# Kernel tuning notes

Measured on AMD Instinct MI355X. Metric: run time of the kernel, lower is better.

Reference implementation:

```python
import jax, jax.numpy as jnp
import numpy as np
from jax import lax

B, N, SEG, T = 64, 19, 15, 400
FIN, HID, K, NH, DM, FF, L, NC = 64, 128, 4, 4, 64, 128, 4, 3
EPS = 1e-5


def setup_inputs() -> dict:
    key = jax.random.key(0)
    ks = jax.random.split(key, 40)
    nrm = lambda i, s, sc=0.05: jax.random.normal(ks[i], s, dtype=jnp.float32) * sc
    inp = {
        "X": jax.random.normal(ks[0], (B, N, SEG, T), dtype=jnp.float32),
        "A_hat": jax.random.uniform(ks[1], (B, K, SEG, N, N), dtype=jnp.float32),
        "conv1_w": nrm(2, (32, 1, 25)), "conv1_b": nrm(3, (32,)),
        "conv2_w": nrm(4, (64, 32, 9)), "conv2_b": nrm(5, (64,)),
        "g1_W": nrm(6, (HID, FIN)), "g1_q": nrm(7, (K,), 1.0),
        "g1_bn_g": jnp.ones((HID,)), "g1_bn_b": jnp.zeros((HID,)),
        "g1_bn_m": jnp.zeros((HID,)), "g1_bn_v": jnp.ones((HID,)),
        "g2_W": nrm(8, (FIN, HID)), "g2_q": nrm(9, (K,), 1.0),
        "g2_bn_g": jnp.ones((FIN,)), "g2_bn_b": jnp.zeros((FIN,)),
        "g2_bn_m": jnp.zeros((FIN,)), "g2_bn_v": jnp.ones((FIN,)),
        "cls_token": nrm(10, (1, 1, DM), 0.02), "pos_emb": nrm(11, (1, SEG + 1, DM), 0.02),
        "t_wqkv": nrm(12, (L, 3 * DM, DM)), "t_bqkv": nrm(13, (L, 3 * DM)),
        "t_wo": nrm(14, (L, DM, DM)), "t_bo": nrm(15, (L, DM)),
        "t_ln1g": jnp.ones((L, DM)), "t_ln1b": jnp.zeros((L, DM)),
        "t_w1": nrm(16, (L, FF, DM)), "t_b1": nrm(17, (L, FF)),
        "t_w2": nrm(18, (L, DM, FF)), "t_b2": nrm(19, (L, DM)),
        "t_ln2g": jnp.ones((L, DM)), "t_ln2b": jnp.zeros((L, DM)),
        "clf_w": nrm(20, (NC, DM)), "clf_b": nrm(21, (NC,)),
    }
    return inp


def _ln(x, g, b):
    mu = x.mean(-1, keepdims=True)
    v = ((x - mu) ** 2).mean(-1, keepdims=True)
    return (x - mu) * lax.rsqrt(v + EPS) * g + b


def _maxpool(x, w):  # x: [M, C, T]
    return lax.reduce_window(x, -jnp.inf, lax.max, (1, 1, w), (1, 1, w), "VALID")


def _temporal_encoder(X, c1w, c1b, c2w, c2b):
    # X: [B, SEG, N, T] -> [B, SEG, N, FIN]
    x = X.reshape(-1, 1, T)
    dn = ("NCH", "OIH", "NCH")
    x = lax.conv_general_dilated(x, c1w, (4,), [(12, 12)], dimension_numbers=dn) + c1b[None, :, None]
    x = _maxpool(jax.nn.relu(x), 4)                      # [M,32,25]
    x = lax.conv_general_dilated(x, c2w, (2,), [(4, 4)], dimension_numbers=dn) + c2b[None, :, None]
    x = _maxpool(jax.nn.relu(x), 2)                      # [M,64,6]
    x = x.mean(-1)                                       # AdaptiveAvgPool1d(1)
    return x.reshape(B, SEG, N, FIN)


def _gcn(Xf, A, W, q, g, b, m, v):
    alpha = jax.nn.softmax(q)                            # [K]
    AX = jnp.einsum("bksnm,bsmf->bksnf", A, Xf)          # K-hop diffusion
    Hk = jnp.einsum("bksnf,of->bksno", AX, W)            # shared linear
    H = jnp.einsum("k,bksno->bsno", alpha, Hk)           # attn-weighted hop mix
    H = (H - m) * lax.rsqrt(v + EPS) * g + b             # eval-mode BatchNorm1d
    return jax.nn.relu(H)


def _forward(X, A_hat, conv1_w, conv1_b, conv2_w, conv2_b,
             g1_W, g1_q, g1_bn_g, g1_bn_b, g1_bn_m, g1_bn_v,
             g2_W, g2_q, g2_bn_g, g2_bn_b, g2_bn_m, g2_bn_v,
             cls_token, pos_emb, t_wqkv, t_bqkv, t_wo, t_bo,
             t_ln1g, t_ln1b, t_w1, t_b1, t_w2, t_b2, t_ln2g, t_ln2b,
             clf_w, clf_b):
    Xs = X.reshape(-1, N, SEG, T).transpose(0, 2, 1, 3)  # [B,SEG,N,T]
    feat = _temporal_encoder(Xs, conv1_w, conv1_b, conv2_w, conv2_b)
    H = _gcn(feat, A_hat, g1_W, g1_q, g1_bn_g, g1_bn_b, g1_bn_m, g1_bn_v)
    H = _gcn(H, A_hat, g2_W, g2_q, g2_bn_g, g2_bn_b, g2_bn_m, g2_bn_v)
    g = H.mean(axis=2)                                   # node-mean -> [B,SEG,DM]
    x = jnp.concatenate([jnp.broadcast_to(cls_token, (B, 1, DM)), g], axis=1)
    x = x + pos_emb[:, : SEG + 1]
    dh = DM // NH
    for l in range(L):
        qkv = x @ t_wqkv[l].T + t_bqkv[l]
        qh, kh, vh = [u.reshape(B, SEG + 1, NH, dh).transpose(0, 2, 1, 3)
                      for u in jnp.split(qkv, 3, axis=-1)]
        attn = jax.nn.softmax(jnp.einsum("bhqd,bhkd->bhqk", qh, kh) / jnp.sqrt(jnp.float32(dh)), axis=-1)
        o = jnp.einsum("bhqk,bhkd->bhqd", attn, vh).transpose(0, 2, 1, 3).reshape(B, SEG + 1, DM)
        x = _ln(x + o @ t_wo[l].T + t_bo[l], t_ln1g[l], t_ln1b[l])
        ff = jax.nn.relu(x @ t_w1[l].T + t_b1[l]) @ t_w2[l].T + t_b2[l]
        x = _ln(x + ff, t_ln2g[l], t_ln2b[l])
    return x[:, 0] @ clf_w.T + clf_b                     # [B, NC]


def reference(X, A_hat, conv1_w, conv1_b, conv2_w, conv2_b,
              g1_W, g1_q, g1_bn_g, g1_bn_b, g1_bn_m, g1_bn_v,
              g2_W, g2_q, g2_bn_g, g2_bn_b, g2_bn_m, g2_bn_v,
              cls_token, pos_emb, t_wqkv, t_bqkv, t_wo, t_bo,
              t_ln1g, t_ln1b, t_w1, t_b1, t_w2, t_b2, t_ln2g, t_ln2b,
              clf_w, clf_b):
    return _forward(X, A_hat, conv1_w, conv1_b, conv2_w, conv2_b,
                    g1_W, g1_q, g1_bn_g, g1_bn_b, g1_bn_m, g1_bn_v,
                    g2_W, g2_q, g2_bn_g, g2_bn_b, g2_bn_m, g2_bn_v,
                    cls_token, pos_emb, t_wqkv, t_bqkv, t_wo, t_bo,
                    t_ln1g, t_ln1b, t_w1, t_b1, t_w2, t_b2, t_ln2g, t_ln2b,
                    clf_w, clf_b)
```

## Files before the change

### kernel.cpp

```cpp
#include <hip/hip_runtime.h>
#include <cmath>

#define B_ 64
#define N_ 19
#define SEG_ 15
#define T_ 400
#define FIN_ 64
#define HID_ 128
#define K_ 4
#define NH_ 4
#define DM_ 64
#define FF_ 128
#define L_ 4
#define NC_ 3
#define EPS_ 1e-5f

typedef __attribute__((ext_vector_type(8))) short bf16x8;
typedef __attribute__((ext_vector_type(4))) short bf16x4;
typedef __attribute__((ext_vector_type(4))) float f32x4;
typedef unsigned short ushort_t;

__device__ __forceinline__ ushort_t f2bf(float x) {
  union { float f; unsigned u; } a; a.f = x;
  unsigned r = a.u + 0x7fffu + ((a.u >> 16) & 1u);
  return (ushort_t)(r >> 16);
}
__device__ __forceinline__ float bf2f(ushort_t h) {
  union { unsigned u; float f; } a; a.u = ((unsigned)h) << 16;
  return a.f;
}

__global__ __launch_bounds__(256) void k_prep(
    const float* __restrict__ c1w, const float* __restrict__ c2w,
    const float* __restrict__ wqkv, const float* __restrict__ wo,
    const float* __restrict__ w1, const float* __restrict__ w2,
    const float* __restrict__ g1W, const float* __restrict__ g2W,
    ushort_t* __restrict__ bt,
    ushort_t* __restrict__ Th, ushort_t* __restrict__ Tl,
    ushort_t* __restrict__ W1h, ushort_t* __restrict__ W1l,
    ushort_t* __restrict__ W2h, ushort_t* __restrict__ W2l,
    ushort_t* __restrict__ C1h, ushort_t* __restrict__ C1l) {
  int gid = blockIdx.x * 256 + threadIdx.x;
  if (gid < 18944) {
    int oc = gid / 296, k = gid - oc * 296;
    int ic = k & 31, kk = k >> 5;
    ushort_t v = 0;
    if (kk < 9) v = f2bf(c2w[oc * 288 + ic * 9 + kk]);
    bt[gid] = v;
  } else if (gid < 68096) {
    int i = gid - 18944;
    int l = i / 12288, r = i % 12288;
    float v = wqkv[i];
    ushort_t h = f2bf(v);
    int dst = l * 32768 + r;
    Th[dst] = h; Tl[dst] = f2bf(v - bf2f(h));
  } else if (gid < 84480) {
    int i = gid - 68096;
    int l = i / 4096, r = i % 4096;
    float v = wo[i];
    ushort_t h = f2bf(v);
    int dst = l * 32768 + 12288 + r;
    Th[dst] = h; Tl[dst] = f2bf(v - bf2f(h));
  } else if (gid < 117248) {
    int i = gid - 84480;
    int l = i / 8192, r = i % 8192;
    float v = w1[i];
    ushort_t h = f2bf(v);
    int dst = l * 32768 + 16384 + r;
    Th[dst] = h; Tl[dst] = f2bf(v - bf2f(h));
  } else if (gid < 150016) {
    int i = gid - 117248;
    int l = i / 8192, r = i % 8192;
    float v = w2[i];
    ushort_t h = f2bf(v);
    int dst = l * 32768 + 24576 + r;
    Th[dst] = h; Tl[dst] = f2bf(v - bf2f(h));
  } else if (gid < 158208) {
    int i = gid - 150016;
    float v = g1W[i];
    ushort_t h = f2bf(v);
    W1h[i] = h;
    W1l[i] = f2bf(v - bf2f(h));
  } else if (gid < 166400) {
    int i = gid - 158208;
    float v = g2W[i];
    ushort_t h = f2bf(v);
    W2h[i] = h;
    W2l[i] = f2bf(v - bf2f(h));
  } else if (gid < 167424) {
    int i = gid - 166400;
    int oc = i >> 5, kk = i & 31;
    float v = (kk < 25) ? c1w[oc * 25 + kk] : 0.f;
    ushort_t h = f2bf(v);
    C1h[i] = h;
    C1l[i] = f2bf(v - bf2f(h));
  }
}

#define RPB 4
#define ICP 40
#define P1R 40
#define OFF_XPH 0
#define OFF_XPL 3840
#define OFF_P1  7680
#define SMEM_T  20480

__global__ __launch_bounds__(256, 4) void k_temporal(
    const float* __restrict__ X, const float* __restrict__ c1b,
    const float* __restrict__ c2b,
    const ushort_t* __restrict__ C1h, const ushort_t* __restrict__ C1l,
    const ushort_t* __restrict__ BmatT, float* __restrict__ Xf) {
  __shared__ __align__(16) unsigned char smem[SMEM_T];
  ushort_t* xph = (ushort_t*)(smem + OFF_XPH);
  ushort_t* xpl = (ushort_t*)(smem + OFF_XPL);
  ushort_t* p1T = (ushort_t*)(smem + OFF_P1);
  float* Dbuf = (float*)smem;

  const int tid = threadIdx.x;
  const int row0 = blockIdx.x * RPB;
  const int lane = tid & 63, wv = tid >> 6;
  const int quad = lane >> 4, nl = lane & 15;

  for (int i = tid; i < 3200; i += 256) ((unsigned*)p1T)[i] = 0u;
  for (int r = 0; r < RPB; ++r) {
    const int gr = row0 + r;
    const int n = gr % N_;
    const int s = (gr / N_) % SEG_;
    const int b = gr / (N_ * SEG_);
    const float* xin = X + (((size_t)b * N_ + n) * SEG_ + s) * T_ - 12;
    for (int i = tid; i < 480; i += 256) {
      float v = (i >= 12 && i < 412) ? xin[i] : 0.f;
      ushort_t h = f2bf(v);
      xph[r * 480 + i] = h;
      xpl[r * 480 + i] = f2bf(v - bf2f(h));
    }
  }
  __syncthreads();

  {
    bf16x8 bh0 = *(const bf16x8*)(C1h + nl * 32 + quad * 8);
    bf16x8 bh1 = *(const bf16x8*)(C1h + (16 + nl) * 32 + quad * 8);
    bf16x8 bl0 = *(const bf16x8*)(C1l + nl * 32 + quad * 8);
    bf16x8 bl1 = *(const bf16x8*)(C1l + (16 + nl) * 32 + quad * 8);
    const float bias0 = c1b[nl], bias1 = c1b[16 + nl];
    for (int t = wv; t < 28; t += 4) {
      const int r = t / 7, mt = t - r * 7;
      const int aoff = r * 480 + mt * 64 + nl * 4 + quad * 8;
      union { bf16x4 q[2]; bf16x8 v; } ah, al;
      ah.q[0] = *(const bf16x4*)(xph + aoff);
      ah.q[1] = *(const bf16x4*)(xph + aoff + 4);
      al.q[0] = *(const bf16x4*)(xpl + aoff);
      al.q[1] = *(const bf16x4*)(xpl + aoff + 4);
      f32x4 a0 = (f32x4){0.f, 0.f, 0.f, 0.f};
      a0 = __builtin_amdgcn_mfma_f32_16x16x32_bf16(ah.v, bh0, a0, 0, 0, 0);
      a0 = __builtin_amdgcn_mfma_f32_16x16x32_bf16(al.v, bh0, a0, 0, 0, 0);
      a0 = __builtin_amdgcn_mfma_f32_16x16x32_bf16(ah.v, bl0, a0, 0, 0, 0);
      f32x4 a1 = (f32x4){0.f, 0.f, 0.f, 0.f};
      a1 = __builtin_amdgcn_mfma_f32_16x16x32_bf16(ah.v, bh1, a1, 0, 0, 0);
      a1 = __builtin_amdgcn_mfma_f32_16x16x32_bf16(al.v, bh1, a1, 0, 0, 0);
      a1 = __builtin_amdgcn_mfma_f32_16x16x32_bf16(ah.v, bl1, a1, 0, 0, 0);
      const int j = mt * 4 + quad;
      if (j < 25) {
        float m0 = fmaxf(fmaxf(a0[0], a0[1]), fmaxf(a0[2], a0[3]));
        float m1 = fmaxf(fmaxf(a1[0], a1[1]), fmaxf(a1[2], a1[3]));
        p1T[(r * P1R + j + 4) * ICP + nl] = f2bf(fmaxf(m0 + bias0, 0.f));
        p1T[(r * P1R + j + 4) * ICP + 16 + nl] = f2bf(fmaxf(m1 + bias1, 0.f));
      }
    }
  }
  __syncthreads();

  f32x4 acc[4];
  int abase[4];
#pragma unroll
  for (int tm = 0; tm < 4; ++tm) {
    acc[tm] = (f32x4){0.f, 0.f, 0.f, 0.f};
    int m = tm * 16 + nl;
    int rl = m / 14;
    int op = m - rl * 14;
    if (rl > 3) rl = 3;
    if (op > 13) op = 13;
    abase[tm] = (rl * P1R + 2 * op) * ICP + quad * 8;
  }
  const ushort_t* brow = BmatT + (wv * 16 + nl) * 296 + quad * 8;
#pragma unroll
  for (int kk = 0; kk < 9; ++kk) {
    bf16x8 bfr = *(const bf16x8*)(brow + kk * 32);
#pragma unroll
    for (int tm = 0; tm < 4; ++tm) {
      bf16x8 afr = *(const bf16x8*)(p1T + abase[tm] + kk * ICP);
      acc[tm] = __builtin_amdgcn_mfma_f32_16x16x32_bf16(afr, bfr, acc[tm], 0, 0, 0);
    }
  }
  __syncthreads();

#pragma unroll
  for (int tm = 0; tm < 4; ++tm)
#pragma unroll
    for (int rg = 0; rg < 4; ++rg)
      Dbuf[(tm * 16 + quad * 4 + rg) * 66 + wv * 16 + nl] = acc[tm][rg];
  __syncthreads();

  for (int o = tid; o < RPB * 64; o += 256) {
    int rl = o >> 6, oc = o & 63;
    float bias = c2b[oc];
    const float* dr = Dbuf + (rl * 14) * 66 + oc;
    float s = 0.f;
#pragma unroll
    for (int jj = 0; jj < 6; ++jj) {
      float v = fmaxf(dr[(2 * jj) * 66], dr[(2 * jj + 1) * 66]) + bias;
      s += fmaxf(v, 0.f);
    }
    Xf[(size_t)(row0 + rl) * FIN_ + oc] = s * (1.f / 6.f);
  }
}

__global__ __launch_bounds__(256) void k_gcn(
    const float* __restrict__ A, const float* __restrict__ Xf,
    const ushort_t* __restrict__ W1h, const ushort_t* __restrict__ W1l,
    const ushort_t* __restrict__ W2h, const ushort_t* __restrict__ W2l,
    const float* __restrict__ q1, const float* __restrict__ q2,
    const float* __restrict__ b1g, const float* __restrict__ b1b,
    const float* __restrict__ b1m, const float* __restrict__ b1v,
    const float* __restrict__ b2g, const float* __restrict__ b2b,
    const float* __restrict__ b2m, const float* __restrict__ b2v,
    float* __restrict__ G) {
  const int bs = blockIdx.x;
  const int b = bs / SEG_;
  const int s = bs % SEG_;
  const int tid = threadIdx.x;

  __shared__ __align__(16) ushort_t xh[32 * 72], xl[32 * 72];
  __shared__ __align__(16) ushort_t Hh[32 * 136], Hl[32 * 136];
  __shared__ float abar1[N_ * N_], abar2[N_ * N_];
  __shared__ float ybuf[N_ * 130];
  __shared__ float zbuf[N_ * 64];
  __shared__ float sc1[HID_], sh1[HID_], sc2[FIN_], sh2[FIN_];

  {
    float p0 = q1[0], p1 = q1[1], p2 = q1[2], p3 = q1[3];
    float mx = fmaxf(fmaxf(p0, p1), fmaxf(p2, p3));
    float e0 = expf(p0 - mx), e1 = expf(p1 - mx), e2 = expf(p2 - mx), e3 = expf(p3 - mx);
    float inv = 1.f / (e0 + e1 + e2 + e3);
    float a0 = e0 * inv, a1 = e1 * inv, a2 = e2 * inv, a3 = e3 * inv;
    float r0 = q2[0], r1 = q2[1], r2 = q2[2], r3 = q2[3];
    float mx2 = fmaxf(fmaxf(r0, r1), fmaxf(r2, r3));
    float f0 = expf(r0 - mx2), f1 = expf(r1 - mx2), f2 = expf(r2 - mx2), f3 = expf(r3 - mx2);
    float inv2 = 1.f / (f0 + f1 + f2 + f3);
    float c0 = f0 * inv2, c1 = f1 * inv2, c2 = f2 * inv2, c3 = f3 * inv2;
    const size_t kstride = (size_t)SEG_ * N_ * N_;
    const float* Ab = A + ((size_t)b * K_ * SEG_ + s) * (N_ * N_);
    for (int i = tid; i < N_ * N_; i += 256) {
      float v0 = Ab[i], v1 = Ab[i + kstride], v2 = Ab[i + 2 * kstride], v3 = Ab[i + 3 * kstride];
      abar1[i] = a0 * v0 + a1 * v1 + a2 * v2 + a3 * v3;
      abar2[i] = c0 * v0 + c1 * v1 + c2 * v2 + c3 * v3;
    }
  }

  for (int i = tid; i < 32 * 72 / 2; i += 256) {
    ((unsigned*)xh)[i] = 0u; ((unsigned*)xl)[i] = 0u;
  }
  for (int i = tid; i < 32 * 136 / 2; i += 256) {
    ((unsigned*)Hh)[i] = 0u; ((unsigned*)Hl)[i] = 0u;
  }
  for (int o = tid; o < HID_; o += 256) {
    float sc = b1g[o] * rsqrtf(b1v[o] + EPS_);
    sc1[o] = sc; sh1[o] = b1b[o] - b1m[o] * sc;
  }
  for (int o = tid; o < FIN_; o += 256) {
    float sc = b2g[o] * rsqrtf(b2v[o] + EPS_);
    sc2[o] = sc; sh2[o] = b2b[o] - b2m[o] * sc;
  }
  __syncthreads();

  const float* xb = Xf + (size_t)bs * N_ * FIN_;
  for (int i = tid; i < N_ * FIN_; i += 256) {
    int r = i >> 6, f = i & 63;
    float v = xb[i];
    ushort_t h = f2bf(v);
    xh[r * 72 + f] = h;
    xl[r * 72 + f] = f2bf(v - bf2f(h));
  }
  __syncthreads();

  const int lane = tid & 63, wv = tid >> 6;
  const int quad = lane >> 4, nl = lane & 15;

#pragma unroll
  for (int mt = 0; mt < 2; ++mt) {
#pragma unroll
    for (int ntl = 0; ntl < 2; ++ntl) {
      const int nt = wv * 2 + ntl;
      f32x4 acc = (f32x4){0.f, 0.f, 0.f, 0.f};
#pragma unroll
      for (int ks = 0; ks < 2; ++ks) {
        bf16x8 ah = *(const bf16x8*)(xh + (mt * 16 + nl) * 72 + ks * 32 + quad * 8);
        bf16x8 al = *(const bf16x8*)(xl + (mt * 16 + nl) * 72 + ks * 32 + quad * 8);
        bf16x8 bh = *(const bf16x8*)(W1h + (nt * 16 + nl) * 64 + ks * 32 + quad * 8);
        bf16x8 bl = *(const bf16x8*)(W1l + (nt * 16 + nl) * 64 + ks * 32 + quad * 8);
        acc = __builtin_amdgcn_mfma_f32_16x16x32_bf16(ah, bh, acc, 0, 0, 0);
        acc = __builtin_amdgcn_mfma_f32_16x16x32_bf16(al, bh, acc, 0, 0, 0);
        acc = __builtin_amdgcn_mfma_f32_16x16x32_bf16(ah, bl, acc, 0, 0, 0);
      }
#pragma unroll
      for (int r = 0; r < 4; ++r) {
        int m = mt * 16 + quad * 4 + r;
        if (m < N_) ybuf[m * 130 + nt * 16 + nl] = acc[r];
      }
    }
  }
  __syncthreads();

  for (int idx = tid; idx < N_ * HID_; idx += 256) {
    int nn = idx >> 7, o = idx & 127;
    float acc = 0.f;
    const float* ar = &abar1[nn * N_];
#pragma unroll
    for (int m = 0; m < N_; ++m) acc += ar[m] * ybuf[m * 130 + o];
    float h = fmaxf(acc * sc1[o] + sh1[o], 0.f);
    ushort_t hh = f2bf(h);
    Hh[nn * 136 + o] = hh;
    Hl[nn * 136 + o] = f2bf(h - bf2f(hh));
  }
  __syncthreads();

  {
    const int nt = wv;
#pragma unroll
    for (int mt = 0; mt < 2; ++mt) {
      f32x4 acc = (f32x4){0.f, 0.f, 0.f, 0.f};
#pragma unroll
      for (int ks = 0; ks < 4; ++ks) {
        bf16x8 ah = *(const bf16x8*)(Hh + (mt * 16 + nl) * 136 + ks * 32 + quad * 8);
        bf16x8 al = *(const bf16x8*)(Hl + (mt * 16 + nl) * 136 + ks * 32 + quad * 8);
        bf16x8 bh = *(const bf16x8*)(W2h + (nt * 16 + nl) * 128 + ks * 32 + quad * 8);
        bf16x8 bl = *(const bf16x8*)(W2l + (nt * 16 + nl) * 128 + ks * 32 + quad * 8);
        acc = __builtin_amdgcn_mfma_f32_16x16x32_bf16(ah, bh, acc, 0, 0, 0);
        acc = __builtin_amdgcn_mfma_f32_16x16x32_bf16(al, bh, acc, 0, 0, 0);
        acc = __builtin_amdgcn_mfma_f32_16x16x32_bf16(ah, bl, acc, 0, 0, 0);
      }
#pragma unroll
      for (int r = 0; r < 4; ++r) {
        int m = mt * 16 + quad * 4 + r;
        if (m < N_) ybuf[m * 66 + nt * 16 + nl] = acc[r];
      }
    }
  }
  __syncthreads();

  for (int idx = tid; idx < N_ * FIN_; idx += 256) {
    int nn = idx >> 6, o = idx & 63;
    float acc = 0.f;
    const float* ar = &abar2[nn * N_];
#pragma unroll
    for (int m = 0; m < N_; ++m) acc += ar[m] * ybuf[m * 66 + o];
    zbuf[idx] = fmaxf(acc * sc2[o] + sh2[o], 0.f);
  }
  __syncthreads();

  if (tid < FIN_) {
    float ssum = 0.f;
#pragma unroll
    for (int nn = 0; nn < N_; ++nn) ssum += zbuf[nn * 64 + tid];
    G[(size_t)bs * FIN_ + tid] = ssum * (1.f / (float)N_);
  }
}

__global__ __launch_bounds__(256, 1) void k_transformer(
    const float* __restrict__ G, const float* __restrict__ cls,
    const float* __restrict__ pos,
    const ushort_t* __restrict__ Th, const ushort_t* __restrict__ Tl,
    const float* __restrict__ bqkv, const float* __restrict__ bo,
    const float* __restrict__ ln1g, const float* __restrict__ ln1b,
    const float* __restrict__ b1, const float* __restrict__ b2,
    const float* __restrict__ ln2g, const float* __restrict__ ln2b,
    const float* __restrict__ clfw, const float* __restrict__ clfb,
    float* __restrict__ out) {
  const int b = blockIdx.x;
  const int tid = threadIdx.x;
  const int lane = tid & 63, wv = tid >> 6;
  const int quad = lane >> 4, nl = lane & 15;

  __shared__ float xbuf[16 * 64];
  __shared__ __align__(16) ushort_t xh[16 * 72], xl[16 * 72];
  __shared__ float qkvb[16 * 196];
  __shared__ float scb[NH_ * 272];
  __shared__ __align__(16) ushort_t oh[16 * 72], ol[16 * 72];
  __shared__ __align__(16) ushort_t h1h[16 * 136], h1l[16 * 136];
  __shared__ float tmpb[16 * 64];

  for (int i = tid; i < 16 * 64; i += 256) {
    int t = i >> 6, d = i & 63;
    float base = (t == 0) ? cls[d] : G[((size_t)b * SEG_ + (t - 1)) * DM_ + d];
    float v = base + pos[t * DM_ + d];
    xbuf[i] = v;
    ushort_t h = f2bf(v);
    xh[t * 72 + d] = h;
    xl[t * 72 + d] = f2bf(v - bf2f(h));
  }
  __syncthreads();

  for (int l = 0; l < L_; ++l) {
    const ushort_t* TH = Th + l * 32768;
    const ushort_t* TL = Tl + l * 32768;

    bf16x8 qwh[3][2], qwl[3][2];
#pragma unroll
    for (int ntl = 0; ntl < 3; ++ntl)
#pragma unroll
      for (int ks = 0; ks < 2; ++ks) {
        const int nt = wv * 3 + ntl;
        qwh[ntl][ks] = *(const bf16x8*)(TH + (nt * 16 + nl) * 64 + ks * 32 + quad * 8);
        qwl[ntl][ks] = *(const bf16x8*)(TL + (nt * 16 + nl) * 64 + ks * 32 + quad * 8);
      }
    bf16x8 owh[2], owl[2];
#pragma unroll
    for (int ks = 0; ks < 2; ++ks) {
      owh[ks] = *(const bf16x8*)(TH + 12288 + (wv * 16 + nl) * 64 + ks * 32 + quad * 8);
      owl[ks] = *(const bf16x8*)(TL + 12288 + (wv * 16 + nl) * 64 + ks * 32 + quad * 8);
    }
    bf16x8 f1h[2][2], f1l[2][2];
#pragma unroll
    for (int ntl = 0; ntl < 2; ++ntl)
#pragma unroll
      for (int ks = 0; ks < 2; ++ks) {
        const int nt = wv * 2 + ntl;
        f1h[ntl][ks] = *(const bf16x8*)(TH + 16384 + (nt * 16 + nl) * 64 + ks * 32 + quad * 8);
        f1l[ntl][ks] = *(const bf16x8*)(TL + 16384 + (nt * 16 + nl) * 64 + ks * 32 + quad * 8);
      }
    bf16x8 f2h[4], f2l[4];
#pragma unroll
    for (int ks = 0; ks < 4; ++ks) {
      f2h[ks] = *(const bf16x8*)(TH + 24576 + (wv * 16 + nl) * 128 + ks * 32 + quad * 8);
      f2l[ks] = *(const bf16x8*)(TL + 24576 + (wv * 16 + nl) * 128 + ks * 32 + quad * 8);
    }

#pragma unroll
    for (int ntl = 0; ntl < 3; ++ntl) {
      const int nt = wv * 3 + ntl;
      f32x4 acc = (f32x4){0.f, 0.f, 0.f, 0.f};
#pragma unroll
      for (int ks = 0; ks < 2; ++ks) {
        bf16x8 ah = *(const bf16x8*)(xh + nl * 72 + ks * 32 + quad * 8);
        bf16x8 al = *(const bf16x8*)(xl + nl * 72 + ks * 32 + quad * 8);
        acc = __builtin_amdgcn_mfma_f32_16x16x32_bf16(ah, qwh[ntl][ks], acc, 0, 0, 0);
        acc = __builtin_amdgcn_mfma_f32_16x16x32_bf16(al, qwh[ntl][ks], acc, 0, 0, 0);
        acc = __builtin_amdgcn_mfma_f32_16x16x32_bf16(ah, qwl[ntl][ks], acc, 0, 0, 0);
      }
      const int j = nt * 16 + nl;
      const float bias = bqkv[l * 192 + j];
#pragma unroll
      for (int r = 0; r < 4; ++r)
        qkvb[(quad * 4 + r) * 196 + j] = acc[r] + bias;
    }
    __syncthreads();

    {
      const int h = wv;
      float sc[4];
      const float* qr = &qkvb[nl * 196 + h * 16];
#pragma unroll
      for (int uu = 0; uu < 4; ++uu) {
        const float* kr = &qkvb[(quad * 4 + uu) * 196 + 64 + h * 16];
        float a = 0.f;
#pragma unroll
        for (int d = 0; d < 16; ++d) a += qr[d] * kr[d];
        sc[uu] = a * 0.25f;
      }
      float mx = fmaxf(fmaxf(sc[0], sc[1]), fmaxf(sc[2], sc[3]));
      mx = fmaxf(mx, __shfl_xor(mx, 16));
      mx = fmaxf(mx, __shfl_xor(mx, 32));
      float e[4];
      float sum = 0.f;
#pragma unroll
      for (int uu = 0; uu < 4; ++uu) { e[uu] = expf(sc[uu] - mx); sum += e[uu]; }
      sum += __shfl_xor(sum, 16);
      sum += __shfl_xor(sum, 32);
      const float is = 1.f / sum;
      float* prow = &scb[h * 272 + nl * 17];
#pragma unroll
      for (int uu = 0; uu < 4; ++uu) prow[quad * 4 + uu] = e[uu] * is;
      float o[4] = {0.f, 0.f, 0.f, 0.f};
      for (int u = 0; u < 16; ++u) {
        float p = prow[u];
        const float* vr = &qkvb[u * 196 + 128 + h * 16 + quad * 4];
#pragma unroll
        for (int dd = 0; dd < 4; ++dd) o[dd] += p * vr[dd];
      }
      const int eb = h * 16 + quad * 4;
#pragma unroll
      for (int dd = 0; dd < 4; ++dd) {
        ushort_t hh = f2bf(o[dd]);
        oh[nl * 72 + eb + dd] = hh;
        ol[nl * 72 + eb + dd] = f2bf(o[dd] - bf2f(hh));
      }
    }
    __syncthreads();

    {
      f32x4 acc = (f32x4){0.f, 0.f, 0.f, 0.f};
#pragma unroll
      for (int ks = 0; ks < 2; ++ks) {
        bf16x8 ah = *(const bf16x8*)(oh + nl * 72 + ks * 32 + quad * 8);
        bf16x8 al = *(const bf16x8*)(ol + nl * 72 + ks * 32 + quad * 8);
        acc = __builtin_amdgcn_mfma_f32_16x16x32_bf16(ah, owh[ks], acc, 0, 0, 0);
        acc = __builtin_amdgcn_mfma_f32_16x16x32_bf16(al, owh[ks], acc, 0, 0, 0);
        acc = __builtin_amdgcn_mfma_f32_16x16x32_bf16(ah, owl[ks], acc, 0, 0, 0);
      }
      const int d = wv * 16 + nl;
      const float bias = bo[l * 64 + d];
#pragma unroll
      for (int r = 0; r < 4; ++r) {
        int t = quad * 4 + r;
        tmpb[t * 64 + d] = xbuf[t * 64 + d] + acc[r] + bias;
      }
    }
    __syncthreads();

    {
      int t = tid >> 4, i2 = tid & 15;
      float4 v = ((const float4*)(tmpb + t * 64))[i2];
      float s = v.x + v.y + v.z + v.w;
      s += __shfl_xor(s, 1); s += __shfl_xor(s, 2);
      s += __shfl_xor(s, 4); s += __shfl_xor(s, 8);
      float mu = s * (1.f / 64.f);
      float d0 = v.x - mu, d1 = v.y - mu, d2 = v.z - mu, d3 = v.w - mu;
      float vr = d0 * d0 + d1 * d1 + d2 * d2 + d3 * d3;
      vr += __shfl_xor(vr, 1); vr += __shfl_xor(vr, 2);
      vr += __shfl_xor(vr, 4); vr += __shfl_xor(vr, 8);
      float rs = rsqrtf(vr * (1.f / 64.f) + EPS_);
      float4 g4 = ((const float4*)(ln1g + l * 64))[i2];
      float4 b4 = ((const float4*)(ln1b + l * 64))[i2];
      float4 o4;
      o4.x = d0 * rs * g4.x + b4.x; o4.y = d1 * rs * g4.y + b4.y;
      o4.z = d2 * rs * g4.z + b4.z; o4.w = d3 * rs * g4.w + b4.w;
      ((float4*)(xbuf + t * 64))[i2] = o4;
      int base = t * 72 + i2 * 4;
      ushort_t h0 = f2bf(o4.x), h1 = f2bf(o4.y), h2 = f2bf(o4.z), h3 = f2bf(o4.w);
      xh[base + 0] = h0; xh[base + 1] = h1; xh[base + 2] = h2; xh[base + 3] = h3;
      xl[base + 0] = f2bf(o4.x - bf2f(h0));
      xl[base + 1] = f2bf(o4.y - bf2f(h1));
      xl[base + 2] = f2bf(o4.z - bf2f(h2));
      xl[base + 3] = f2bf(o4.w - bf2f(h3));
    }
    __syncthreads();

#pragma unroll
    for (int ntl = 0; ntl < 2; ++ntl) {
      const int nt = wv * 2 + ntl;
      f32x4 acc = (f32x4){0.f, 0.f, 0.f, 0.f};
#pragma unroll
      for (int ks = 0; ks < 2; ++ks) {
        bf16x8 ah = *(const bf16x8*)(xh + nl * 72 + ks * 32 + quad * 8);
        bf16x8 al = *(const bf16x8*)(xl + nl * 72 + ks * 32 + quad * 8);
        acc = __builtin_amdgcn_mfma_f32_16x16x32_bf16(ah, f1h[ntl][ks], acc, 0, 0, 0);
        acc = __builtin_amdgcn_mfma_f32_16x16x32_bf16(al, f1h[ntl][ks], acc, 0, 0, 0);
        acc = __builtin_amdgcn_mfma_f32_16x16x32_bf16(ah, f1l[ntl][ks], acc, 0, 0, 0);
      }
      const int f = nt * 16 + nl;
      const float bias = b1[l * 128 + f];
#pragma unroll
      for (int r = 0; r < 4; ++r) {
        int t = quad * 4 + r;
        float v = fmaxf(acc[r] + bias, 0.f);
        ushort_t hh = f2bf(v);
        h1h[t * 136 + f] = hh;
        h1l[t * 136 + f] = f2bf(v - bf2f(hh));
      }
    }
    __syncthreads();

    {
      f32x4 acc = (f32x4){0.f, 0.f, 0.f, 0.f};
#pragma unroll
      for (int ks = 0; ks < 4; ++ks) {
        bf16x8 ah = *(const bf16x8*)(h1h + nl * 136 + ks * 32 + quad * 8);
        bf16x8 al = *(const bf16x8*)(h1l + nl * 136 + ks * 32 + quad * 8);
        acc = __builtin_amdgcn_mfma_f32_16x16x32_bf16(ah, f2h[ks], acc, 0, 0, 0);
        acc = __builtin_amdgcn_mfma_f32_16x16x32_bf16(al, f2h[ks], acc, 0, 0, 0);
        acc = __builtin_amdgcn_mfma_f32_16x16x32_bf16(ah, f2l[ks], acc, 0, 0, 0);
      }
      const int d = wv * 16 + nl;
      const float bias = b2[l * 64 + d];
#pragma unroll
      for (int r = 0; r < 4; ++r) {
        int t = quad * 4 + r;
        tmpb[t * 64 + d] = xbuf[t * 64 + d] + acc[r] + bias;
      }
    }
    __syncthreads();

    {
      int t = tid >> 4, i2 = tid & 15;
      float4 v = ((const float4*)(tmpb + t * 64))[i2];
      float s = v.x + v.y + v.z + v.w;
      s += __shfl_xor(s, 1); s += __shfl_xor(s, 2);
      s += __shfl_xor(s, 4); s += __shfl_xor(s, 8);
      float mu = s * (1.f / 64.f);
      float d0 = v.x - mu, d1 = v.y - mu, d2 = v.z - mu, d3 = v.w - mu;
      float vr = d0 * d0 + d1 * d1 + d2 * d2 + d3 * d3;
      vr += __shfl_xor(vr, 1); vr += __shfl_xor(vr, 2);
      vr += __shfl_xor(vr, 4); vr += __shfl_xor(vr, 8);
      float rs = rsqrtf(vr * (1.f / 64.f) + EPS_);
      float4 g4 = ((const float4*)(ln2g + l * 64))[i2];
      float4 b4 = ((const float4*)(ln2b + l * 64))[i2];
      float4 o4;
      o4.x = d0 * rs * g4.x + b4.x; o4.y = d1 * rs * g4.y + b4.y;
      o4.z = d2 * rs * g4.z + b4.z; o4.w = d3 * rs * g4.w + b4.w;
      ((float4*)(xbuf + t * 64))[i2] = o4;
      int base = t * 72 + i2 * 4;
      ushort_t h0 = f2bf(o4.x), h1 = f2bf(o4.y), h2 = f2bf(o4.z), h3 = f2bf(o4.w);
      xh[base + 0] = h0; xh[base + 1] = h1; xh[base + 2] = h2; xh[base + 3] = h3;
      xl[base + 0] = f2bf(o4.x - bf2f(h0));
      xl[base + 1] = f2bf(o4.y - bf2f(h1));
      xl[base + 2] = f2bf(o4.z - bf2f(h2));
      xl[base + 3] = f2bf(o4.w - bf2f(h3));
    }
    __syncthreads();
  }

  if (tid < NC_) {
    float acc = clfb[tid];
    const float* wr = &clfw[tid * DM_];
    for (int d = 0; d < DM_; ++d) acc += xbuf[d] * wr[d];
    out[b * NC_ + tid] = acc;
  }
}

extern "C" void kernel_launch(void* const* d_in, const int* in_sizes, int n_in,
                              void* d_out, int out_size, void* d_ws, size_t ws_size,
                              hipStream_t stream) {
  (void)in_sizes; (void)n_in; (void)out_size; (void)ws_size;
  const float* X    = (const float*)d_in[0];
  const float* A    = (const float*)d_in[1];
  const float* c1w  = (const float*)d_in[2];
  const float* c1b  = (const float*)d_in[3];
  const float* c2w  = (const float*)d_in[4];
  const float* c2b  = (const float*)d_in[5];
  const float* g1W  = (const float*)d_in[6];
  const float* g1q  = (const float*)d_in[7];
  const float* g1g  = (const float*)d_in[8];
  const float* g1b  = (const float*)d_in[9];
  const float* g1m  = (const float*)d_in[10];
  const float* g1v  = (const float*)d_in[11];
  const float* g2W  = (const float*)d_in[12];
  const float* g2q  = (const float*)d_in[13];
  const float* g2g  = (const float*)d_in[14];
  const float* g2b  = (const float*)d_in[15];
  const float* g2m  = (const float*)d_in[16];
  const float* g2v  = (const float*)d_in[17];
  const float* cls  = (const float*)d_in[18];
  const float* pos  = (const float*)d_in[19];
  const float* wqkv = (const float*)d_in[20];
  const float* bqkv = (const float*)d_in[21];
  const float* wo   = (const float*)d_in[22];
  const float* bo   = (const float*)d_in[23];
  const float* ln1g = (const float*)d_in[24];
  const float* ln1b = (const float*)d_in[25];
  const float* w1   = (const float*)d_in[26];
  const float* b1   = (const float*)d_in[27];
  const float* w2   = (const float*)d_in[28];
  const float* b2   = (const float*)d_in[29];
  const float* ln2g = (const float*)d_in[30];
  const float* ln2b = (const float*)d_in[31];
  const float* clfw = (const float*)d_in[32];
  const float* clfb = (const float*)d_in[33];
  float* out = (float*)d_out;

  char* wsb = (char*)d_ws;
  ushort_t* BmatT = (ushort_t*)(wsb + 0);
  ushort_t* Th  = (ushort_t*)(wsb + 37888);
  ushort_t* Tl  = (ushort_t*)(wsb + 300032);
  ushort_t* W1h = (ushort_t*)(wsb + 562176);
  ushort_t* W1l = (ushort_t*)(wsb + 578560);
  ushort_t* W2h = (ushort_t*)(wsb + 594944);
  ushort_t* W2l = (ushort_t*)(wsb + 611328);
  ushort_t* C1h = (ushort_t*)(wsb + 627712);
  ushort_t* C1l = (ushort_t*)(wsb + 629760);
  float* Xf   = (float*)(wsb + 631808);
  float* G    = (float*)(wsb + 5301248);

  k_prep<<<654, 256, 0, stream>>>(c1w, c2w, wqkv, wo, w1, w2, g1W, g2W,
                                  BmatT, Th, Tl, W1h, W1l, W2h, W2l, C1h, C1l);
  k_temporal<<<B_ * SEG_ * N_ / RPB, 256, 0, stream>>>(
      X, c1b, c2b, C1h, C1l, BmatT, Xf);
  k_gcn<<<B_ * SEG_, 256, 0, stream>>>(A, Xf, W1h, W1l, W2h, W2l,
                                       g1q, g2q, g1g, g1b, g1m, g1v,
                                       g2g, g2b, g2m, g2v, G);
  k_transformer<<<B_, 256, 0, stream>>>(G, cls, pos, Th, Tl,
                                        bqkv, bo, ln1g, ln1b, b1, b2, ln2g, ln2b,
                                        clfw, clfb, out);
}
```

Measured before the change: 216.3 us.

## Run GCN adjacency aggregation on MFMA and stage transformer params in LDS

The GCN kernel now computes the per-segment adjacency aggregations (Abar·Y) with split-bf16 MFMA instead of scalar FP32 loops. To do this it builds transposed bf16 hi/lo copies of the weighted adjacency and of the intermediate features in LDS, and reorders the weight GEMMs to produce a transposed output. It also requests two blocks per CU. Separately, the transformer kernel preloads all per-layer biases, layernorm params and classifier weights into shared memory once instead of reading them from global memory inside each layer. The split-bf16 scheme adds rounding error on the adjacency and intermediate products.

```diff
diff --git a/kernel.cpp b/kernel.cpp
--- a/kernel.cpp
+++ b/kernel.cpp
@@ -215,7 +215,7 @@
   }
 }
 
-__global__ __launch_bounds__(256) void k_gcn(
+__global__ __launch_bounds__(256, 2) void k_gcn(
     const float* __restrict__ A, const float* __restrict__ Xf,
     const ushort_t* __restrict__ W1h, const ushort_t* __restrict__ W1l,
     const ushort_t* __restrict__ W2h, const ushort_t* __restrict__ W2l,
@@ -229,13 +229,36 @@
   const int b = bs / SEG_;
   const int s = bs % SEG_;
   const int tid = threadIdx.x;
+  const int lane = tid & 63, wv = tid >> 6;
+  const int quad = lane >> 4, nl = lane & 15;
 
   __shared__ __align__(16) ushort_t xh[32 * 72], xl[32 * 72];
   __shared__ __align__(16) ushort_t Hh[32 * 136], Hl[32 * 136];
-  __shared__ float abar1[N_ * N_], abar2[N_ * N_];
-  __shared__ float ybuf[N_ * 130];
+  __shared__ __align__(16) ushort_t a1h[32 * 40], a1l[32 * 40];
+  __shared__ __align__(16) ushort_t a2h[32 * 40], a2l[32 * 40];
+  __shared__ __align__(16) ushort_t yTh[128 * 40], yTl[128 * 40];
   __shared__ float zbuf[N_ * 64];
   __shared__ float sc1[HID_], sh1[HID_], sc2[FIN_], sh2[FIN_];
+
+  for (int i = tid; i < 32 * 72 / 2; i += 256) {
+    ((unsigned*)xh)[i] = 0u; ((unsigned*)xl)[i] = 0u;
+  }
+  for (int i = tid; i < 32 * 136 / 2; i += 256) {
+    ((unsigned*)Hh)[i] = 0u; ((unsigned*)Hl)[i] = 0u;
+  }
+  for (int i = tid; i < 32 * 40 / 2; i += 256) {
+    ((unsigned*)a1h)[i] = 0u; ((unsigned*)a1l)[i] = 0u;
+    ((unsigned*)a2h)[i] = 0u; ((unsigned*)a2l)[i] = 0u;
+  }
+  for (int o = tid; o < HID_; o += 256) {
+    float sc = b1g[o] * rsqrtf(b1v[o] + EPS_);
+    sc1[o] = sc; sh1[o] = b1b[o] - b1m[o] * sc;
+  }
+  for (int o = tid; o < FIN_; o += 256) {
+    float sc = b2g[o] * rsqrtf(b2v[o] + EPS_);
+    sc2[o] = sc; sh2[o] = b2b[o] - b2m[o] * sc;
+  }
+  __syncthreads();
 
   {
     float p0 = q1[0], p1 = q1[1], p2 = q1[2], p3 = q1[3];
@@ -251,40 +274,55 @@
     const size_t kstride = (size_t)SEG_ * N_ * N_;
     const float* Ab = A + ((size_t)b * K_ * SEG_ + s) * (N_ * N_);
     for (int i = tid; i < N_ * N_; i += 256) {
+      int n = i / N_, m = i - n * N_;
       float v0 = Ab[i], v1 = Ab[i + kstride], v2 = Ab[i + 2 * kstride], v3 = Ab[i + 3 * kstride];
-      abar1[i] = a0 * v0 + a1 * v1 + a2 * v2 + a3 * v3;
-      abar2[i] = c0 * v0 + c1 * v1 + c2 * v2 + c3 * v3;
-    }
-  }
-
-  for (int i = tid; i < 32 * 72 / 2; i += 256) {
-    ((unsigned*)xh)[i] = 0u; ((unsigned*)xl)[i] = 0u;
-  }
-  for (int i = tid; i < 32 * 136 / 2; i += 256) {
-    ((unsigned*)Hh)[i] = 0u; ((unsigned*)Hl)[i] = 0u;
-  }
-  for (int o = tid; o < HID_; o += 256) {
-    float sc = b1g[o] * rsqrtf(b1v[o] + EPS_);
-    sc1[o] = sc; sh1[o] = b1b[o] - b1m[o] * sc;
-  }
-  for (int o = tid; o < FIN_; o += 256) {
-    float sc = b2g[o] * rsqrtf(b2v[o] + EPS_);
-    sc2[o] = sc; sh2[o] = b2b[o] - b2m[o] * sc;
-  }
-  __syncthreads();
-
-  const float* xb = Xf + (size_t)bs * N_ * FIN_;
-  for (int i = tid; i < N_ * FIN_; i += 256) {
-    int r = i >> 6, f = i & 63;
-    float v = xb[i];
-    ushort_t h = f2bf(v);
-    xh[r * 72 + f] = h;
-    xl[r * 72 + f] = f2bf(v - bf2f(h));
-  }
-  __syncthreads();
-
-  const int lane = tid & 63, wv = tid >> 6;
-  const int quad = lane >> 4, nl = lane & 15;
+      float w1v = a0 * v0 + a1 * v1 + a2 * v2 + a3 * v3;
+      float w2v = c0 * v0 + c1 * v1 + c2 * v2 + c3 * v3;
+      ushort_t h1 = f2bf(w1v);
+      a1h[n * 40 + m] = h1; a1l[n * 40 + m] = f2bf(w1v - bf2f(h1));
+      ushort_t h2 = f2bf(w2v);
+      a2h[n * 40 + m] = h2; a2l[n * 40 + m] = f2bf(w2v - bf2f(h2));
+    }
+  }
+  {
+    const float* xb = Xf + (size_t)bs * N_ * FIN_;
+    for (int i = tid; i < N_ * FIN_; i += 256) {
+      int r = i >> 6, f = i & 63;
+      float v = xb[i];
+      ushort_t h = f2bf(v);
+      xh[r * 72 + f] = h;
+      xl[r * 72 + f] = f2bf(v - bf2f(h));
+    }
+  }
+  __syncthreads();
+
+#pragma unroll
+  for (int mtl = 0; mtl < 2; ++mtl) {
+    const int om = (wv * 2 + mtl) * 16;
+#pragma unroll
+    for (int nt = 0; nt < 2; ++nt) {
+      f32x4 acc = (f32x4){0.f, 0.f, 0.f, 0.f};
+#pragma unroll
+      for (int ks = 0; ks < 2; ++ks) {
+        bf16x8 ah = *(const bf16x8*)(W1h + (om + nl) * 64 + ks * 32 + quad * 8);
+        bf16x8 al = *(const bf16x8*)(W1l + (om + nl) * 64 + ks * 32 + quad * 8);
+        bf16x8 bh = *(const bf16x8*)(xh + (nt * 16 + nl) * 72 + ks * 32 + quad * 8);
+        bf16x8 bl = *(const bf16x8*)(xl + (nt * 16 + nl) * 72 + ks * 32 + quad * 8);
+        acc = __builtin_amdgcn_mfma_f32_16x16x32_bf16(ah, bh, acc, 0, 0, 0);
+        acc = __builtin_amdgcn_mfma_f32_16x16x32_bf16(al, bh, acc, 0, 0, 0);
+        acc = __builtin_amdgcn_mfma_f32_16x16x32_bf16(ah, bl, acc, 0, 0, 0);
+      }
+#pragma unroll
+      for (int r = 0; r < 4; ++r) {
+        int o = om + quad * 4 + r, node = nt * 16 + nl;
+        float v = acc[r];
+        ushort_t hh = f2bf(v);
+        yTh[o * 40 + node] = hh;
+        yTl[o * 40 + node] = f2bf(v - bf2f(hh));
+      }
+    }
+  }
+  __syncthreads();
 
 #pragma unroll
   for (int mt = 0; mt < 2; ++mt) {
@@ -292,69 +330,74 @@
     for (int ntl = 0; ntl < 2; ++ntl) {
       const int nt = wv * 2 + ntl;
       f32x4 acc = (f32x4){0.f, 0.f, 0.f, 0.f};
-#pragma unroll
-      for (int ks = 0; ks < 2; ++ks) {
-        bf16x8 ah = *(const bf16x8*)(xh + (mt * 16 + nl) * 72 + ks * 32 + quad * 8);
-        bf16x8 al = *(const bf16x8*)(xl + (mt * 16 + nl) * 72 + ks * 32 + quad * 8);
-        bf16x8 bh = *(const bf16x8*)(W1h + (nt * 16 + nl) * 64 + ks * 32 + quad * 8);
-        bf16x8 bl = *(const bf16x8*)(W1l + (nt * 16 + nl) * 64 + ks * 32 + quad * 8);
+      bf16x8 ah = *(const bf16x8*)(a1h + (mt * 16 + nl) * 40 + quad * 8);
+      bf16x8 al = *(const bf16x8*)(a1l + (mt * 16 + nl) * 40 + quad * 8);
+      bf16x8 bh = *(const bf16x8*)(yTh + (nt * 16 + nl) * 40 + quad * 8);
+      bf16x8 bl = *(const bf16x8*)(yTl + (nt * 16 + nl) * 40 + quad * 8);
+      acc = __builtin_amdgcn_mfma_f32_16x16x32_bf16(ah, bh, acc, 0, 0, 0);
+      acc = __builtin_amdgcn_mfma_f32_16x16x32_bf16(al, bh, acc, 0, 0, 0);
+      acc = __builtin_amdgcn_mfma_f32_16x16x32_bf16(ah, bl, acc, 0, 0, 0);
+      const int o = nt * 16 + nl;
+      const float sc = sc1[o], sh = sh1[o];
+#pragma unroll
+      for (int r = 0; r < 4; ++r) {
+        int node = mt * 16 + quad * 4 + r;
+        if (node < N_) {
+          float h = fmaxf(acc[r] * sc + sh, 0.f);
+          ushort_t hh = f2bf(h);
+          Hh[node * 136 + o] = hh;
+          Hl[node * 136 + o] = f2bf(h - bf2f(hh));
+        }
+      }
+    }
+  }
+  __syncthreads();
+
+  {
+    const int om = wv * 16;
+#pragma unroll
+    for (int nt = 0; nt < 2; ++nt) {
+      f32x4 acc = (f32x4){0.f, 0.f, 0.f, 0.f};
+#pragma unroll
+      for (int ks = 0; ks < 4; ++ks) {
+        bf16x8 ah = *(const bf16x8*)(W2h + (om + nl) * 128 + ks * 32 + quad * 8);
+        bf16x8 al = *(const bf16x8*)(W2l + (om + nl) * 128 + ks * 32 + quad * 8);
+        bf16x8 bh = *(const bf16x8*)(Hh + (nt * 16 + nl) * 136 + ks * 32 + quad * 8);
+        bf16x8 bl = *(const bf16x8*)(Hl + (nt * 16 + nl) * 136 + ks * 32 + quad * 8);
         acc = __builtin_amdgcn_mfma_f32_16x16x32_bf16(ah, bh, acc, 0, 0, 0);
         acc = __builtin_amdgcn_mfma_f32_16x16x32_bf16(al, bh, acc, 0, 0, 0);
         acc = __builtin_amdgcn_mfma_f32_16x16x32_bf16(ah, bl, acc, 0, 0, 0);
       }
 #pragma unroll
       for (int r = 0; r < 4; ++r) {
-        int m = mt * 16 + quad * 4 + r;
-        if (m < N_) ybuf[m * 130 + nt * 16 + nl] = acc[r];
-      }
-    }
-  }
-  __syncthreads();
-
-  for (int idx = tid; idx < N_ * HID_; idx += 256) {
-    int nn = idx >> 7, o = idx & 127;
-    float acc = 0.f;
-    const float* ar = &abar1[nn * N_];
-#pragma unroll
-    for (int m = 0; m < N_; ++m) acc += ar[m] * ybuf[m * 130 + o];
-    float h = fmaxf(acc * sc1[o] + sh1[o], 0.f);
-    ushort_t hh = f2bf(h);
-    Hh[nn * 136 + o] = hh;
-    Hl[nn * 136 + o] = f2bf(h - bf2f(hh));
-  }
-  __syncthreads();
-
-  {
-    const int nt = wv;
-#pragma unroll
-    for (int mt = 0; mt < 2; ++mt) {
-      f32x4 acc = (f32x4){0.f, 0.f, 0.f, 0.f};
-#pragma unroll
-      for (int ks = 0; ks < 4; ++ks) {
-        bf16x8 ah = *(const bf16x8*)(Hh + (mt * 16 + nl) * 136 + ks * 32 + quad * 8);
-        bf16x8 al = *(const bf16x8*)(Hl + (mt * 16 + nl) * 136 + ks * 32 + quad * 8);
-        bf16x8 bh = *(const bf16x8*)(W2h + (nt * 16 + nl) * 128 + ks * 32 + quad * 8);
-        bf16x8 bl = *(const bf16x8*)(W2l + (nt * 16 + nl) * 128 + ks * 32 + quad * 8);
-        acc = __builtin_amdgcn_mfma_f32_16x16x32_bf16(ah, bh, acc, 0, 0, 0);
-        acc = __builtin_amdgcn_mfma_f32_16x16x32_bf16(al, bh, acc, 0, 0, 0);
-        acc = __builtin_amdgcn_mfma_f32_16x16x32_bf16(ah, bl, acc, 0, 0, 0);
-      }
-#pragma unroll
-      for (int r = 0; r < 4; ++r) {
-        int m = mt * 16 + quad * 4 + r;
-        if (m < N_) ybuf[m * 66 + nt * 16 + nl] = acc[r];
-      }
-    }
-  }
-  __syncthreads();
-
-  for (int idx = tid; idx < N_ * FIN_; idx += 256) {
-    int nn = idx >> 6, o = idx & 63;
-    float acc = 0.f;
-    const float* ar = &abar2[nn * N_];
-#pragma unroll
-    for (int m = 0; m < N_; ++m) acc += ar[m] * ybuf[m * 66 + o];
-    zbuf[idx] = fmaxf(acc * sc2[o] + sh2[o], 0.f);
+        int o2 = om + quad * 4 + r, node = nt * 16 + nl;
+        float v = acc[r];
+        ushort_t hh = f2bf(v);
+        yTh[o2 * 40 + node] = hh;
+        yTl[o2 * 40 + node] = f2bf(v - bf2f(hh));
+      }
+    }
+  }
+  __syncthreads();
+
+#pragma unroll
+  for (int mt = 0; mt < 2; ++mt) {
+    f32x4 acc = (f32x4){0.f, 0.f, 0.f, 0.f};
+    bf16x8 ah = *(const bf16x8*)(a2h + (mt * 16 + nl) * 40 + quad * 8);
+    bf16x8 al = *(const bf16x8*)(a2l + (mt * 16 + nl) * 40 + quad * 8);
+    bf16x8 bh = *(const bf16x8*)(yTh + (wv * 16 + nl) * 40 + quad * 8);
+    bf16x8 bl = *(const bf16x8*)(yTl + (wv * 16 + nl) * 40 + quad * 8);
+    acc = __builtin_amdgcn_mfma_f32_16x16x32_bf16(ah, bh, acc, 0, 0, 0);
+    acc = __builtin_amdgcn_mfma_f32_16x16x32_bf16(al, bh, acc, 0, 0, 0);
+    acc = __builtin_amdgcn_mfma_f32_16x16x32_bf16(ah, bl, acc, 0, 0, 0);
+    const int o2 = wv * 16 + nl;
+    const float sc = sc2[o2], sh = sh2[o2];
+#pragma unroll
+    for (int r = 0; r < 4; ++r) {
+      int node = mt * 16 + quad * 4 + r;
+      if (node < N_)
+        zbuf[node * 64 + o2] = fmaxf(acc[r] * sc + sh, 0.f);
+    }
   }
   __syncthreads();
 
@@ -388,6 +431,24 @@
   __shared__ __align__(16) ushort_t oh[16 * 72], ol[16 * 72];
   __shared__ __align__(16) ushort_t h1h[16 * 136], h1l[16 * 136];
   __shared__ float tmpb[16 * 64];
+  __shared__ __align__(16) float pbuf[L_ * 704];
+  __shared__ __align__(16) float cw[200];
+
+  for (int i = tid; i < L_ * 704; i += 256) {
+    int l = i / 704, r = i - l * 704;
+    float v;
+    if (r < 192)       v = bqkv[l * 192 + r];
+    else if (r < 256)  v = bo[l * 64 + r - 192];
+    else if (r < 384)  v = b1[l * 128 + r - 256];
+    else if (r < 448)  v = b2[l * 64 + r - 384];
+    else if (r < 512)  v = ln1g[l * 64 + r - 448];
+    else if (r < 576)  v = ln1b[l * 64 + r - 512];
+    else if (r < 640)  v = ln2g[l * 64 + r - 576];
+    else               v = ln2b[l * 64 + r - 640];
+    pbuf[i] = v;
+  }
+  if (tid < 192) cw[tid] = clfw[tid];
+  if (tid < NC_) cw[192 + tid] = clfb[tid];
 
   for (int i = tid; i < 16 * 64; i += 256) {
     int t = i >> 6, d = i & 63;
@@ -403,6 +464,7 @@
   for (int l = 0; l < L_; ++l) {
     const ushort_t* TH = Th + l * 32768;
     const ushort_t* TL = Tl + l * 32768;
+    const float* P = pbuf + l * 704;
 
     bf16x8 qwh[3][2], qwl[3][2];
 #pragma unroll
@@ -448,7 +510,7 @@
         acc = __builtin_amdgcn_mfma_f32_16x16x32_bf16(ah, qwl[ntl][ks], acc, 0, 0, 0);
       }
       const int j = nt * 16 + nl;
-      const float bias = bqkv[l * 192 + j];
+      const float bias = P[j];
 #pragma unroll
       for (int r = 0; r < 4; ++r)
         qkvb[(quad * 4 + r) * 196 + j] = acc[r] + bias;
@@ -508,7 +570,7 @@
         acc = __builtin_amdgcn_mfma_f32_16x16x32_bf16(ah, owl[ks], acc, 0, 0, 0);
       }
       const int d = wv * 16 + nl;
-      const float bias = bo[l * 64 + d];
+      const float bias = P[192 + d];
 #pragma unroll
       for (int r = 0; r < 4; ++r) {
         int t = quad * 4 + r;
@@ -529,8 +591,8 @@
       vr += __shfl_xor(vr, 1); vr += __shfl_xor(vr, 2);
       vr += __shfl_xor(vr, 4); vr += __shfl_xor(vr, 8);
       float rs = rsqrtf(vr * (1.f / 64.f) + EPS_);
-      float4 g4 = ((const float4*)(ln1g + l * 64))[i2];
-      float4 b4 = ((const float4*)(ln1b + l * 64))[i2];
+      float4 g4 = ((const float4*)(P + 448))[i2];
+      float4 b4 = ((const float4*)(P + 512))[i2];
       float4 o4;
       o4.x = d0 * rs * g4.x + b4.x; o4.y = d1 * rs * g4.y + b4.y;
       o4.z = d2 * rs * g4.z + b4.z; o4.w = d3 * rs * g4.w + b4.w;
@@ -558,7 +620,7 @@
         acc = __builtin_amdgcn_mfma_f32_16x16x32_bf16(ah, f1l[ntl][ks], acc, 0, 0, 0);
       }
       const int f = nt * 16 + nl;
-      const float bias = b1[l * 128 + f];
+      const float bias = P[256 + f];
 #pragma unroll
       for (int r = 0; r < 4; ++r) {
         int t = quad * 4 + r;
@@ -581,7 +643,7 @@
         acc = __builtin_amdgcn_mfma_f32_16x16x32_bf16(ah, f2l[ks], acc, 0, 0, 0);
       }
       const int d = wv * 16 + nl;
-      const float bias = b2[l * 64 + d];
+      const float bias = P[384 + d];
 #pragma unroll
       for (int r = 0; r < 4; ++r) {
         int t = quad * 4 + r;
@@ -602,8 +664,8 @@
       vr += __shfl_xor(vr, 1); vr += __shfl_xor(vr, 2);
       vr += __shfl_xor(vr, 4); vr += __shfl_xor(vr, 8);
       float rs = rsqrtf(vr * (1.f / 64.f) + EPS_);
-      float4 g4 = ((const float4*)(ln2g + l * 64))[i2];
-      float4 b4 = ((const float4*)(ln2b + l * 64))[i2];
+      float4 g4 = ((const float4*)(P + 576))[i2];
+      float4 b4 = ((const float4*)(P + 640))[i2];
       float4 o4;
       o4.x = d0 * rs * g4.x + b4.x; o4.y = d1 * rs * g4.y + b4.y;
       o4.z = d2 * rs * g4.z + b4.z; o4.w = d3 * rs * g4.w + b4.w;
@@ -620,8 +682,8 @@
   }
 
   if (tid < NC_) {
-    float acc = clfb[tid];
-    const float* wr = &clfw[tid * DM_];
+    float acc = cw[192 + tid];
+    const float* wr = &cw[tid * DM_];
     for (int d = 0; d < DM_; ++d) acc += xbuf[d] * wr[d];
     out[b * NC_ + tid] = acc;
   }
```

Measured after the change: 221.8 us. 2.5% more time.
